# Optimization experiments

Measured on AMD Instinct MI355X. Metric: run time of the kernel, lower is better.

The kernel has to match this reference:

```python
import jax, jax.numpy as jnp
import numpy as np

LEAKY_ALPHA = 0.2  # LeakyReLU negative slope from init arg `alpha`


def setup_inputs() -> dict:
    key = jax.random.key(0)
    k1, k2, k3, k4 = jax.random.split(key, 4)
    B, N, Fin, Fout = 8, 2048, 256, 256
    h = jax.random.normal(k1, (B, N, Fin), dtype=jnp.float32)
    adj = jax.random.randint(k2, (N, N), 0, 2, dtype=jnp.int32)
    W = jax.random.normal(k3, (Fin, Fout), dtype=jnp.float32) * (1.414 * (6.0 / (Fin + Fout)) ** 0.5)
    a = jax.random.normal(k4, (2 * Fout, 1), dtype=jnp.float32) * (1.414 * (6.0 / (2 * Fout + 1)) ** 0.5)
    return {"h": h, "adj": adj, "W": W, "a": a}


def reference(h, adj, W, a):
    # h: (B, N, Fin), adj: (N, N) int {0,1}, W: (Fin, Fout), a: (2*Fout, 1)
    Fout = W.shape[1]
    Wh = jnp.einsum('bnf,fo->bno', h, W)            # (B, N, Fout)
    a1 = a[:Fout, 0]                                  # attends to target node i
    a2 = a[Fout:, 0]                                  # attends to source node j
    # a^T [Wh_i || Wh_j] == (Wh_i . a1) + (Wh_j . a2); LeakyReLU applied after, as in original
    s_i = Wh @ a1                                     # (B, N)
    s_j = Wh @ a2                                     # (B, N)
    e = jax.nn.leaky_relu(s_i[:, :, None] + s_j[:, None, :], negative_slope=LEAKY_ALPHA)  # (B, N, N)
    N = Wh.shape[1]
    mask = (adj > 0) | jnp.eye(N, dtype=bool)         # adjacency + self-loops
    e = jnp.where(mask[None, :, :], e, -jnp.inf)
    attention = jax.nn.softmax(e, axis=-1)            # dropout is identity in eval
    attention = jnp.nan_to_num(attention, nan=0.0)
    h_prime = jnp.einsum('bij,bjo->bio', attention, Wh)  # (B, N, Fout)
    return jax.nn.elu(h_prime)                        # concat=True -> ELU
```

## Files before the change

### kernel.cpp

```cpp
#include <hip/hip_runtime.h>

typedef unsigned short u16;
typedef unsigned int   u32;
typedef unsigned long long u64;

typedef __bf16 bf16x8 __attribute__((ext_vector_type(8)));
typedef float  f32x4  __attribute__((ext_vector_type(4)));

#define MFMA_BF16(a,b,c) __builtin_amdgcn_mfma_f32_16x16x32_bf16((a),(b),(c),0,0,0)

__device__ __forceinline__ float bf2f(u16 u) {
    return __uint_as_float(((u32)u) << 16);
}
__device__ __forceinline__ u16 f2bf(float x) {
    u32 u = __float_as_uint(x);
    u += 0x7fffu + ((u >> 16) & 1u);
    return (u16)(u >> 16);
}
__device__ __forceinline__ float ldany(const void* p, size_t i, int f32) {
    return f32 ? ((const float*)p)[i] : bf2f(((const u16*)p)[i]);
}
__device__ __forceinline__ int detect_f32(const u32* hw) {
    u32 w = hw[threadIdx.x & 63];
    int e = (w >> 23) & 0xFF;
    u64 m = __ballot(e >= 64 && e <= 190);
    return __popcll(m) >= 32 ? 1 : 0;
}

__global__ __launch_bounds__(256) void k0(const void* __restrict__ w, const void* __restrict__ a,
                                          u16* __restrict__ wt, float* __restrict__ wa1,
                                          float* __restrict__ wa2, const u32* __restrict__ hw) {
    int f32 = detect_f32(hw);
    int k = blockIdx.x, o = threadIdx.x;
    float wv = ldany(w, (size_t)k * 256 + o, f32);
    wt[o * 256 + k] = f2bf(wv);
    float p1 = wv * ldany(a, o, f32);
    float p2 = wv * ldany(a, 256 + o, f32);
    for (int d = 32; d; d >>= 1) { p1 += __shfl_down(p1, d); p2 += __shfl_down(p2, d); }
    __shared__ float s1[4], s2[4];
    int wid = o >> 6, lane = o & 63;
    if (lane == 0) { s1[wid] = p1; s2[wid] = p2; }
    __syncthreads();
    if (o == 0) { wa1[k] = s1[0] + s1[1] + s1[2] + s1[3]; wa2[k] = s2[0] + s2[1] + s2[2] + s2[3]; }
}

__global__ __launch_bounds__(256) void k1m(const int* __restrict__ adj, u64* __restrict__ mb64) {
    int t = threadIdx.x;
    int wv = t >> 6, lane = t & 63;
    #pragma unroll
    for (int q = 0; q < 4; q++) {
        int idx = blockIdx.x * 16 + wv * 4 + q;
        int mrow = idx >> 5, c = idx & 31;
        int j = c * 64 + lane;
        bool bit = (adj[(size_t)mrow * 2048 + j] > 0) || (j == mrow);
        u64 m = __ballot(bit);
        if (lane == 0) mb64[(size_t)mrow * 32 + c] = m;
    }
}

struct __align__(16) K2LDS {
    u16 At[64 * 68];
    union { u16 Bt[256 * 68]; u16 Ct[256 * 68]; };
    float wa1s[256], wa2s[256];
    float s1[64], s2[64];
};
__global__ __launch_bounds__(256) void k2(const void* __restrict__ h, const u16* __restrict__ wt,
                                          const float* __restrict__ wa1, const float* __restrict__ wa2,
                                          u16* __restrict__ whbt,
                                          float* __restrict__ sig, float* __restrict__ sjg) {
    __shared__ K2LDS L;
    int f32 = detect_f32((const u32*)h);
    int m0 = blockIdx.x * 64;
    int b  = m0 >> 11;
    int n0 = m0 & 2047;
    int t = threadIdx.x;
    int wid = t >> 6, lane = t & 63, ln = lane & 15, qd = lane >> 4;

    L.wa1s[t] = wa1[t]; L.wa2s[t] = wa2[t];
    if (t < 64) { L.s1[t] = 0.f; L.s2[t] = 0.f; }
    __syncthreads();

    float a1lo = 0.f, a2lo = 0.f, a1hi = 0.f, a2hi = 0.f;

    f32x4 acc[4][4];
    for (int mi = 0; mi < 4; mi++)
        for (int ni = 0; ni < 4; ni++)
            acc[mi][ni] = (f32x4){0.f, 0.f, 0.f, 0.f};

    for (int c = 0; c < 4; c++) {
        int k0c = c * 64;
        for (int p = 0; p < 2; p++) {
            int r = (t >> 3) + p * 32, s = t & 7;
            float xv[8]; u16 uv[8];
            if (f32) {
                const float* src = (const float*)h + (size_t)(m0 + r) * 256 + k0c + s * 8;
                f32x4 x0 = *(const f32x4*)src;
                f32x4 x1 = *(const f32x4*)(src + 4);
                #pragma unroll
                for (int q = 0; q < 4; q++) { xv[q] = x0[q]; xv[4 + q] = x1[q]; }
                #pragma unroll
                for (int q = 0; q < 8; q++) uv[q] = f2bf(xv[q]);
            } else {
                const u16* src = (const u16*)h + (size_t)(m0 + r) * 256 + k0c + s * 8;
                *(uint4*)uv = *(const uint4*)src;
                #pragma unroll
                for (int q = 0; q < 8; q++) xv[q] = bf2f(uv[q]);
            }
            *(uint4*)&L.At[r * 68 + s * 8] = *(uint4*)uv;
            float pa = 0.f, pb = 0.f;
            #pragma unroll
            for (int q = 0; q < 8; q++) {
                pa += xv[q] * L.wa1s[k0c + s * 8 + q];
                pb += xv[q] * L.wa2s[k0c + s * 8 + q];
            }
            if (p == 0) { a1lo += pa; a2lo += pb; } else { a1hi += pa; a2hi += pb; }
        }
        for (int p = 0; p < 8; p++) {
            int f = (t >> 3) + p * 32, s = t & 7;
            *(uint4*)&L.Bt[f * 68 + s * 8] =
                *(const uint4*)(wt + (size_t)f * 256 + k0c + s * 8);
        }
        __syncthreads();
        for (int ks = 0; ks < 2; ks++) {
            bf16x8 af[4], bfr[4];
            for (int mi = 0; mi < 4; mi++)
                af[mi] = *(const bf16x8*)&L.At[(mi * 16 + ln) * 68 + ks * 32 + qd * 8];
            for (int ni = 0; ni < 4; ni++)
                bfr[ni] = *(const bf16x8*)&L.Bt[(wid * 64 + ni * 16 + ln) * 68 + ks * 32 + qd * 8];
            for (int mi = 0; mi < 4; mi++)
                for (int ni = 0; ni < 4; ni++)
                    acc[mi][ni] = MFMA_BF16(af[mi], bfr[ni], acc[mi][ni]);
        }
        __syncthreads();
    }

    atomicAdd(&L.s1[t >> 3], a1lo);        atomicAdd(&L.s2[t >> 3], a2lo);
    atomicAdd(&L.s1[(t >> 3) + 32], a1hi); atomicAdd(&L.s2[(t >> 3) + 32], a2hi);

    for (int mi = 0; mi < 4; mi++) {
        for (int ni = 0; ni < 4; ni++) {
            int f = wid * 64 + ni * 16 + ln;
            int n = mi * 16 + qd * 4;
            u16 v[4];
            for (int r = 0; r < 4; r++) v[r] = f2bf(acc[mi][ni][r]);
            *(uint2*)&L.Ct[f * 68 + n] = *(uint2*)v;
        }
    }
    __syncthreads();
    if (t < 64) { sig[m0 + t] = L.s1[t]; sjg[m0 + t] = L.s2[t]; }
    {
        int fr = t;
        size_t base = (size_t)b * 524288 + (size_t)fr * 2048 + n0;
        #pragma unroll
        for (int s = 0; s < 8; s++) {
            uint4 v = *(uint4*)&L.Ct[fr * 68 + s * 8];
            *(uint4*)(whbt + base + s * 8) = v;
        }
    }
}

__global__ __launch_bounds__(512) void k3n(const float* __restrict__ sig, const float* __restrict__ sjg,
                                           float* __restrict__ u1g, float* __restrict__ u2g,
                                           u32* __restrict__ vpackg, u16* __restrict__ sjbfg) {
    int b = blockIdx.x;
    int t = threadIdx.x;
    const float* sjb = sjg + (size_t)b * 2048;
    float mx = -3.4e38f;
    #pragma unroll
    for (int p = 0; p < 4; p++) mx = fmaxf(mx, sjb[t + p * 512]);
    for (int d = 32; d; d >>= 1) mx = fmaxf(mx, __shfl_xor(mx, d));
    __shared__ float wmax[8];
    int wid = t >> 6, lane = t & 63;
    if (lane == 0) wmax[wid] = mx;
    __syncthreads();
    float Mb = fmaxf(fmaxf(fmaxf(wmax[0], wmax[1]), fmaxf(wmax[2], wmax[3])),
                     fmaxf(fmaxf(wmax[4], wmax[5]), fmaxf(wmax[6], wmax[7])));
    #pragma unroll
    for (int p = 0; p < 4; p++) {
        int j = t + p * 512;
        float sjv = sjb[j];
        float vj  = __expf(sjv - Mb);
        float v2j = __expf(0.2f * (sjv - Mb));
        vpackg[b * 2048 + j] = (u32)f2bf(vj) | ((u32)f2bf(v2j) << 16);
        sjbfg[b * 2048 + j]  = f2bf(sjv);
        float siv = sig[b * 2048 + j];
        float x = siv + Mb;
        float K = fmaxf(x, 0.2f * x);
        u1g[b * 2048 + j] = __expf(x - K);
        u2g[b * 2048 + j] = __expf(0.2f * x - K);
    }
}

struct __align__(16) K4LDS {
    u32   vpack[2048];
    u16   sjb[2048];
    u64   mw[64 * 33];
    float u1[64], u2[64], nsi[64], inv[64];
    float lred[512];
    u16   Pt[2][4096];
    int   claim[2];
};
__global__ __launch_bounds__(512, 1) void k4(const float* __restrict__ sig,
                                             const float* __restrict__ u1g, const float* __restrict__ u2g,
                                             const u32* __restrict__ vpackg, const u16* __restrict__ sjbfg,
                                             const u64* __restrict__ mb64, const u16* __restrict__ whbt,
                                             void* __restrict__ out, const void* __restrict__ hdet,
                                             int* __restrict__ cnt) {
    __shared__ K4LDS L;
    int f32 = detect_f32((const u32*)hdet);
    int t = threadIdx.x;
    if (t == 0) {
        int xcd = __builtin_amdgcn_s_getreg(63508) & 7;
        int bsel = 0, tile = 0;
        #pragma unroll
        for (int k = 0; k < 8; k++) {
            int bb = (xcd + k) & 7;
            int tt = atomicAdd(&cnt[bb], 1);
            if (tt < 32) { bsel = bb; tile = tt; break; }
        }
        L.claim[0] = bsel; L.claim[1] = tile;
    }
    __syncthreads();
    int b  = L.claim[0];
    int i0 = L.claim[1] * 64;
    int wid = t >> 6, lane = t & 63, ln = lane & 15, qd = lane >> 4;
    const u16* wb = whbt + (size_t)b * 524288 + (size_t)wid * 32 * 2048;
    float lacc = 0.f;

    bf16x8 br[2][4];
    #define LOAD_B(cc, bb) do {                                             \
        int j0_ = (cc) * 64;                                                \
        _Pragma("unroll")                                                   \
        for (int ni = 0; ni < 2; ni++)                                      \
            _Pragma("unroll")                                               \
            for (int ks = 0; ks < 2; ks++)                                  \
                br[bb][ni * 2 + ks] = *(const bf16x8*)(wb +                 \
                    (size_t)(ni * 16 + ln) * 2048 + j0_ + ks * 32 + qd * 8);\
    } while (0)

    #define PGEN(cc, bb) do {                                               \
        int r_ = lane, o_ = wid;                                            \
        int jb_ = (cc) * 64 + o_ * 8;                                       \
        uint4 pkA_ = *(const uint4*)&L.vpack[jb_];                          \
        uint4 pkB_ = *(const uint4*)&L.vpack[jb_ + 4];                      \
        uint4 sj4_ = *(const uint4*)&L.sjb[jb_];                            \
        u32 mb_ = (u32)(L.mw[r_ * 33 + (cc)] >> (o_ * 8)) & 0xffu;          \
        float u1_ = L.u1[r_], u2_ = L.u2[r_], nsi_ = L.nsi[r_];             \
        u32 pr_[4];                                                         \
        _Pragma("unroll")                                                   \
        for (int pk = 0; pk < 4; pk++) {                                    \
            u32 vw0_ = (pk == 0) ? pkA_.x : (pk == 1) ? pkA_.z              \
                     : (pk == 2) ? pkB_.x : pkB_.z;                         \
            u32 vw1_ = (pk == 0) ? pkA_.y : (pk == 1) ? pkA_.w              \
                     : (pk == 2) ? pkB_.y : pkB_.w;                         \
            u32 sw_ = (pk == 0) ? sj4_.x : (pk == 1) ? sj4_.y               \
                     : (pk == 2) ? sj4_.z : sj4_.w;                         \
            float sj0_ = __uint_as_float(sw_ << 16);                        \
            float sj1_ = __uint_as_float(sw_ & 0xffff0000u);                \
            float p0_, p1_;                                                 \
            {                                                               \
                bool pos = sj0_ > nsi_;                                     \
                float vv = __uint_as_float(pos ? (vw0_ << 16)               \
                                               : ((vw0_ >> 16) << 16));     \
                p0_ = (pos ? u1_ : u2_) * vv;                               \
                p0_ = ((mb_ >> (2 * pk)) & 1u) ? p0_ : 0.f;                 \
            }                                                               \
            {                                                               \
                bool pos = sj1_ > nsi_;                                     \
                float vv = __uint_as_float(pos ? (vw1_ << 16)               \
                                               : ((vw1_ >> 16) << 16));     \
                p1_ = (pos ? u1_ : u2_) * vv;                               \
                p1_ = ((mb_ >> (2 * pk + 1)) & 1u) ? p1_ : 0.f;             \
            }                                                               \
            lacc += p0_ + p1_;                                              \
            pr_[pk] = __builtin_amdgcn_perm(__float_as_uint(p1_),           \
                                            __float_as_uint(p0_),           \
                                            0x07060302u);                   \
        }                                                                   \
        *(uint4*)&L.Pt[bb][t * 8] = *(uint4*)pr_;                           \
    } while (0)

    LOAD_B(0, 0);
    for (int p = 0; p < 4; p++) { int idx = t + p * 512; L.vpack[idx] = vpackg[b * 2048 + idx]; }
    for (int p = 0; p < 2; p++) { int idx = t + p * 512;
        ((u32*)L.sjb)[idx] = ((const u32*)(sjbfg + (size_t)b * 2048))[idx]; }
    for (int p = 0; p < 4; p++) {
        int idx = t + p * 512;
        int r = idx >> 5, c = idx & 31;
        L.mw[r * 33 + c] = mb64[(size_t)(i0 + r) * 32 + c];
    }
    if (t < 64) {
        int row = b * 2048 + i0 + t;
        L.u1[t] = u1g[row]; L.u2[t] = u2g[row]; L.nsi[t] = -sig[row];
    }
    __syncthreads();
    PGEN(0, 0);

    f32x4 acc[4][2];
    for (int mi = 0; mi < 4; mi++)
        for (int ni = 0; ni < 2; ni++)
            acc[mi][ni] = (f32x4){0.f, 0.f, 0.f, 0.f};

    #define STEP(c, cur, nxt) do {                                          \
        __syncthreads();                                                    \
        if ((c) < 31) { LOAD_B((c) + 1, nxt); PGEN((c) + 1, nxt); }         \
        _Pragma("unroll")                                                   \
        for (int ks = 0; ks < 2; ks++) {                                    \
            bf16x8 af[4];                                                   \
            _Pragma("unroll")                                               \
            for (int mi = 0; mi < 4; mi++)                                  \
                af[mi] = *(const bf16x8*)&L.Pt[cur][((ks * 4 + qd) * 64 +   \
                                                     mi * 16 + ln) * 8];    \
            _Pragma("unroll")                                               \
            for (int mi = 0; mi < 4; mi++)                                  \
                _Pragma("unroll")                                           \
                for (int ni = 0; ni < 2; ni++)                              \
                    acc[mi][ni] = MFMA_BF16(af[mi], br[cur][ni * 2 + ks],   \
                                            acc[mi][ni]);                   \
        }                                                                   \
    } while (0)

    for (int cc = 0; cc < 16; cc++) {
        STEP(2 * cc,     0, 1);
        STEP(2 * cc + 1, 1, 0);
    }

    __syncthreads();
    L.lred[t] = lacc;
    __syncthreads();
    if (t < 64) {
        float s = 0.f;
        #pragma unroll
        for (int q = 0; q < 8; q++) s += L.lred[q * 64 + t];
        L.inv[t] = 1.0f / s;
    }
    __syncthreads();

    for (int mi = 0; mi < 4; mi++) {
        for (int ni = 0; ni < 2; ni++) {
            int fg = wid * 32 + ni * 16 + ln;
            for (int reg = 0; reg < 4; reg++) {
                int rl = mi * 16 + qd * 4 + reg;
                float hp = acc[mi][ni][reg] * L.inv[rl];
                float y = hp > 0.f ? hp : (__expf(hp) - 1.f);
                size_t idx = (size_t)(b * 2048 + i0 + rl) * 256 + fg;
                if (f32) ((float*)out)[idx] = y;
                else     ((u16*)out)[idx]   = f2bf(y);
            }
        }
    }
    #undef LOAD_B
    #undef PGEN
    #undef STEP
}

extern "C" void kernel_launch(void* const* d_in, const int* in_sizes, int n_in,
                              void* d_out, int out_size, void* d_ws, size_t ws_size,
                              hipStream_t stream) {
    const void* h   = d_in[0];
    const int*  adj = (const int*)d_in[1];
    const void* W   = d_in[2];
    const void* a   = d_in[3];

    char* ws = (char*)d_ws;
    u16*   WT    = (u16*)  (ws + 0);
    float* si    = (float*)(ws + 131072);
    float* sj    = (float*)(ws + 196608);
    float* u1    = (float*)(ws + 262144);
    float* u2    = (float*)(ws + 327680);
    u32*   vpack = (u32*)  (ws + 458752);
    u16*   sjbf  = (u16*)  (ws + 524288);
    u64*   mb64  = (u64*)  (ws + 557056);
    u16*   whbt  = (u16*)  (ws + 1081344);
    float* Wa1   = (float*)(ws + 9469952);
    float* Wa2   = (float*)(ws + 9470976);
    int*   cnt   = (int*)  (ws + 9472000);

    hipMemsetAsync(cnt, 0, 32, stream);
    k0 <<<dim3(256),  dim3(256), 0, stream>>>(W, a, WT, Wa1, Wa2, (const u32*)h);
    k1m<<<dim3(4096), dim3(256), 0, stream>>>(adj, mb64);
    k2 <<<dim3(256),  dim3(256), 0, stream>>>(h, WT, Wa1, Wa2, whbt, si, sj);
    k3n<<<dim3(8),    dim3(512), 0, stream>>>(si, sj, u1, u2, vpack, sjbf);
    k4 <<<dim3(256),  dim3(512), 0, stream>>>(si, u1, u2, vpack, sjbf, mb64, whbt, d_out, h, cnt);
}
```

Baseline: 139.5 us.

## Generate attention tiles in registers per wave, drop LDS staging and block syncs

The aggregation kernel now runs 256 threads per block. Each wave owns 32 rows and half of the feature columns, and builds its bf16 attention A-fragments directly in registers from global vpack, sj and mask data. This removes the LDS P tile, the shared staging arrays and the per-chunk __syncthreads. Softmax denominators are reduced with wave shuffles instead of through shared memory. In exchange, each wave redundantly computes the P values for its rows (two waves per row group), holds a much larger B-fragment register set, and issues more global loads with fewer threads per block.

```diff
diff --git a/kernel.cpp b/kernel.cpp
--- a/kernel.cpp
+++ b/kernel.cpp
@@ -191,22 +191,21 @@
     }
 }
 
-struct __align__(16) K4LDS {
-    u32   vpack[2048];
-    u16   sjb[2048];
-    u64   mw[64 * 33];
-    float u1[64], u2[64], nsi[64], inv[64];
-    float lred[512];
-    u16   Pt[2][4096];
-    int   claim[2];
-};
-__global__ __launch_bounds__(512, 1) void k4(const float* __restrict__ sig,
+__device__ __forceinline__ float pval(u32 vw, float sjv, float nsi,
+                                      float u1v, float u2v, u32 mbit) {
+    bool pos = sjv > nsi;
+    float vv = __uint_as_float(pos ? (vw << 16) : (vw & 0xffff0000u));
+    float uu = pos ? u1v : u2v;
+    float p = uu * vv;
+    return mbit ? p : 0.f;
+}
+__global__ __launch_bounds__(256, 1) void k4(const float* __restrict__ sig,
                                              const float* __restrict__ u1g, const float* __restrict__ u2g,
                                              const u32* __restrict__ vpackg, const u16* __restrict__ sjbfg,
                                              const u64* __restrict__ mb64, const u16* __restrict__ whbt,
                                              void* __restrict__ out, const void* __restrict__ hdet,
                                              int* __restrict__ cnt) {
-    __shared__ K4LDS L;
+    __shared__ int claim2[2];
     int f32 = detect_f32((const u32*)hdet);
     int t = threadIdx.x;
     if (t == 0) {
@@ -218,140 +217,124 @@
             int tt = atomicAdd(&cnt[bb], 1);
             if (tt < 32) { bsel = bb; tile = tt; break; }
         }
-        L.claim[0] = bsel; L.claim[1] = tile;
-    }
-    __syncthreads();
-    int b  = L.claim[0];
-    int i0 = L.claim[1] * 64;
+        claim2[0] = bsel; claim2[1] = tile;
+    }
+    __syncthreads();
+    int b  = claim2[0];
+    int i0 = claim2[1] * 64;
     int wid = t >> 6, lane = t & 63, ln = lane & 15, qd = lane >> 4;
-    const u16* wb = whbt + (size_t)b * 524288 + (size_t)wid * 32 * 2048;
-    float lacc = 0.f;
-
-    bf16x8 br[2][4];
-    #define LOAD_B(cc, bb) do {                                             \
-        int j0_ = (cc) * 64;                                                \
+    int rg = wid >> 1, fh = wid & 1;
+
+    int gi = b * 2048 + i0 + rg * 32;
+    const u16* wb = whbt + (size_t)b * 524288 + (size_t)(fh * 128) * 2048;
+    const u32* vp  = vpackg + (size_t)b * 2048;
+    const u16* sjp = sjbfg + (size_t)b * 2048;
+    const u64* mwr0 = mb64 + (size_t)(i0 + rg * 32 + ln) * 32;
+    const u64* mwr1 = mwr0 + 16 * 32;
+
+    float u1_0 = u1g[gi + ln],      u1_1 = u1g[gi + 16 + ln];
+    float u2_0 = u2g[gi + ln],      u2_1 = u2g[gi + 16 + ln];
+    float nsi0 = -sig[gi + ln],     nsi1 = -sig[gi + 16 + ln];
+    float lacc0 = 0.f, lacc1 = 0.f;
+
+    bf16x8 br[16];
+    bf16x8 ar[4];
+
+    #define LOAD_B_KS(cc, ks) do {                                          \
         _Pragma("unroll")                                                   \
-        for (int ni = 0; ni < 2; ni++)                                      \
-            _Pragma("unroll")                                               \
-            for (int ks = 0; ks < 2; ks++)                                  \
-                br[bb][ni * 2 + ks] = *(const bf16x8*)(wb +                 \
-                    (size_t)(ni * 16 + ln) * 2048 + j0_ + ks * 32 + qd * 8);\
+        for (int ni = 0; ni < 8; ni++)                                      \
+            br[ni * 2 + (ks)] = *(const bf16x8*)(wb +                       \
+                (size_t)(ni * 16 + ln) * 2048 + (cc) * 64 + (ks) * 32 + qd * 8);\
     } while (0)
 
-    #define PGEN(cc, bb) do {                                               \
-        int r_ = lane, o_ = wid;                                            \
-        int jb_ = (cc) * 64 + o_ * 8;                                       \
-        uint4 pkA_ = *(const uint4*)&L.vpack[jb_];                          \
-        uint4 pkB_ = *(const uint4*)&L.vpack[jb_ + 4];                      \
-        uint4 sj4_ = *(const uint4*)&L.sjb[jb_];                            \
-        u32 mb_ = (u32)(L.mw[r_ * 33 + (cc)] >> (o_ * 8)) & 0xffu;          \
-        float u1_ = L.u1[r_], u2_ = L.u2[r_], nsi_ = L.nsi[r_];             \
-        u32 pr_[4];                                                         \
-        _Pragma("unroll")                                                   \
-        for (int pk = 0; pk < 4; pk++) {                                    \
-            u32 vw0_ = (pk == 0) ? pkA_.x : (pk == 1) ? pkA_.z              \
-                     : (pk == 2) ? pkB_.x : pkB_.z;                         \
-            u32 vw1_ = (pk == 0) ? pkA_.y : (pk == 1) ? pkA_.w              \
-                     : (pk == 2) ? pkB_.y : pkB_.w;                         \
-            u32 sw_ = (pk == 0) ? sj4_.x : (pk == 1) ? sj4_.y               \
-                     : (pk == 2) ? sj4_.z : sj4_.w;                         \
-            float sj0_ = __uint_as_float(sw_ << 16);                        \
-            float sj1_ = __uint_as_float(sw_ & 0xffff0000u);                \
-            float p0_, p1_;                                                 \
-            {                                                               \
-                bool pos = sj0_ > nsi_;                                     \
-                float vv = __uint_as_float(pos ? (vw0_ << 16)               \
-                                               : ((vw0_ >> 16) << 16));     \
-                p0_ = (pos ? u1_ : u2_) * vv;                               \
-                p0_ = ((mb_ >> (2 * pk)) & 1u) ? p0_ : 0.f;                 \
-            }                                                               \
-            {                                                               \
-                bool pos = sj1_ > nsi_;                                     \
-                float vv = __uint_as_float(pos ? (vw1_ << 16)               \
-                                               : ((vw1_ >> 16) << 16));     \
-                p1_ = (pos ? u1_ : u2_) * vv;                               \
-                p1_ = ((mb_ >> (2 * pk + 1)) & 1u) ? p1_ : 0.f;             \
-            }                                                               \
-            lacc += p0_ + p1_;                                              \
-            pr_[pk] = __builtin_amdgcn_perm(__float_as_uint(p1_),           \
-                                            __float_as_uint(p0_),           \
-                                            0x07060302u);                   \
-        }                                                                   \
-        *(uint4*)&L.Pt[bb][t * 8] = *(uint4*)pr_;                           \
-    } while (0)
-
-    LOAD_B(0, 0);
-    for (int p = 0; p < 4; p++) { int idx = t + p * 512; L.vpack[idx] = vpackg[b * 2048 + idx]; }
-    for (int p = 0; p < 2; p++) { int idx = t + p * 512;
-        ((u32*)L.sjb)[idx] = ((const u32*)(sjbfg + (size_t)b * 2048))[idx]; }
-    for (int p = 0; p < 4; p++) {
-        int idx = t + p * 512;
-        int r = idx >> 5, c = idx & 31;
-        L.mw[r * 33 + c] = mb64[(size_t)(i0 + r) * 32 + c];
-    }
-    if (t < 64) {
-        int row = b * 2048 + i0 + t;
-        L.u1[t] = u1g[row]; L.u2[t] = u2g[row]; L.nsi[t] = -sig[row];
-    }
-    __syncthreads();
-    PGEN(0, 0);
-
-    f32x4 acc[4][2];
-    for (int mi = 0; mi < 4; mi++)
-        for (int ni = 0; ni < 2; ni++)
-            acc[mi][ni] = (f32x4){0.f, 0.f, 0.f, 0.f};
-
-    #define STEP(c, cur, nxt) do {                                          \
-        __syncthreads();                                                    \
-        if ((c) < 31) { LOAD_B((c) + 1, nxt); PGEN((c) + 1, nxt); }         \
+    #define PGEN(cc) do {                                                   \
+        u64 mw0_ = mwr0[cc], mw1_ = mwr1[cc];                               \
         _Pragma("unroll")                                                   \
         for (int ks = 0; ks < 2; ks++) {                                    \
-            bf16x8 af[4];                                                   \
+            int jb_ = (cc) * 64 + ks * 32 + qd * 8;                         \
+            u32 vv_[8];                                                     \
+            *(uint4*)&vv_[0] = *(const uint4*)&vp[jb_];                     \
+            *(uint4*)&vv_[4] = *(const uint4*)&vp[jb_ + 4];                 \
+            u32 sw_[4];                                                     \
+            *(uint4*)sw_ = *(const uint4*)&sjp[jb_];                        \
+            u32 mB0_ = (u32)(mw0_ >> (ks * 32 + qd * 8)) & 0xffu;           \
+            u32 mB1_ = (u32)(mw1_ >> (ks * 32 + qd * 8)) & 0xffu;           \
+            u32 pk0_[4], pk1_[4];                                           \
             _Pragma("unroll")                                               \
-            for (int mi = 0; mi < 4; mi++)                                  \
-                af[mi] = *(const bf16x8*)&L.Pt[cur][((ks * 4 + qd) * 64 +   \
-                                                     mi * 16 + ln) * 8];    \
-            _Pragma("unroll")                                               \
-            for (int mi = 0; mi < 4; mi++)                                  \
-                _Pragma("unroll")                                           \
-                for (int ni = 0; ni < 2; ni++)                              \
-                    acc[mi][ni] = MFMA_BF16(af[mi], br[cur][ni * 2 + ks],   \
-                                            acc[mi][ni]);                   \
+            for (int pk = 0; pk < 4; pk++) {                                \
+                float sj0_ = __uint_as_float(sw_[pk] << 16);                \
+                float sj1_ = __uint_as_float(sw_[pk] & 0xffff0000u);        \
+                float a0_ = pval(vv_[2 * pk],     sj0_, nsi0, u1_0, u2_0,   \
+                                 (mB0_ >> (2 * pk)) & 1u);                  \
+                float a1_ = pval(vv_[2 * pk + 1], sj1_, nsi0, u1_0, u2_0,   \
+                                 (mB0_ >> (2 * pk + 1)) & 1u);              \
+                lacc0 += a0_ + a1_;                                         \
+                pk0_[pk] = __builtin_amdgcn_perm(__float_as_uint(a1_),      \
+                                                 __float_as_uint(a0_),      \
+                                                 0x07060302u);              \
+                float b0_ = pval(vv_[2 * pk],     sj0_, nsi1, u1_1, u2_1,   \
+                                 (mB1_ >> (2 * pk)) & 1u);                  \
+                float b1_ = pval(vv_[2 * pk + 1], sj1_, nsi1, u1_1, u2_1,   \
+                                 (mB1_ >> (2 * pk + 1)) & 1u);              \
+                lacc1 += b0_ + b1_;                                         \
+                pk1_[pk] = __builtin_amdgcn_perm(__float_as_uint(b1_),      \
+                                                 __float_as_uint(b0_),      \
+                                                 0x07060302u);              \
+            }                                                               \
+            ar[ks]     = *(bf16x8*)pk0_;                                    \
+            ar[2 + ks] = *(bf16x8*)pk1_;                                    \
         }                                                                   \
     } while (0)
 
-    for (int cc = 0; cc < 16; cc++) {
-        STEP(2 * cc,     0, 1);
-        STEP(2 * cc + 1, 1, 0);
-    }
-
-    __syncthreads();
-    L.lred[t] = lacc;
-    __syncthreads();
-    if (t < 64) {
-        float s = 0.f;
-        #pragma unroll
-        for (int q = 0; q < 8; q++) s += L.lred[q * 64 + t];
-        L.inv[t] = 1.0f / s;
-    }
-    __syncthreads();
-
-    for (int mi = 0; mi < 4; mi++) {
-        for (int ni = 0; ni < 2; ni++) {
-            int fg = wid * 32 + ni * 16 + ln;
-            for (int reg = 0; reg < 4; reg++) {
-                int rl = mi * 16 + qd * 4 + reg;
-                float hp = acc[mi][ni][reg] * L.inv[rl];
+    f32x4 acc0[8], acc1[8];
+    #pragma unroll
+    for (int ni = 0; ni < 8; ni++) {
+        acc0[ni] = (f32x4){0.f, 0.f, 0.f, 0.f};
+        acc1[ni] = (f32x4){0.f, 0.f, 0.f, 0.f};
+    }
+
+    LOAD_B_KS(0, 0);
+    LOAD_B_KS(0, 1);
+    PGEN(0);
+
+    for (int c = 0; c < 32; c++) {
+        #pragma unroll
+        for (int ni = 0; ni < 8; ni++) {
+            acc0[ni] = MFMA_BF16(ar[0], br[ni * 2 + 0], acc0[ni]);
+            acc1[ni] = MFMA_BF16(ar[2], br[ni * 2 + 0], acc1[ni]);
+        }
+        if (c < 31) LOAD_B_KS(c + 1, 0);
+        #pragma unroll
+        for (int ni = 0; ni < 8; ni++) {
+            acc0[ni] = MFMA_BF16(ar[1], br[ni * 2 + 1], acc0[ni]);
+            acc1[ni] = MFMA_BF16(ar[3], br[ni * 2 + 1], acc1[ni]);
+        }
+        if (c < 31) { LOAD_B_KS(c + 1, 1); PGEN(c + 1); }
+    }
+
+    lacc0 += __shfl_xor(lacc0, 16); lacc0 += __shfl_xor(lacc0, 32);
+    lacc1 += __shfl_xor(lacc1, 16); lacc1 += __shfl_xor(lacc1, 32);
+    float linv0 = 1.0f / lacc0, linv1 = 1.0f / lacc1;
+
+    #pragma unroll
+    for (int mi = 0; mi < 2; mi++) {
+        #pragma unroll
+        for (int reg = 0; reg < 4; reg++) {
+            float inv = __shfl(mi ? linv1 : linv0, qd * 4 + reg);
+            int row = b * 2048 + i0 + rg * 32 + mi * 16 + qd * 4 + reg;
+            #pragma unroll
+            for (int ni = 0; ni < 8; ni++) {
+                int fg = fh * 128 + ni * 16 + ln;
+                float hp = (mi ? acc1[ni][reg] : acc0[ni][reg]) * inv;
                 float y = hp > 0.f ? hp : (__expf(hp) - 1.f);
-                size_t idx = (size_t)(b * 2048 + i0 + rl) * 256 + fg;
+                size_t idx = (size_t)row * 256 + fg;
                 if (f32) ((float*)out)[idx] = y;
                 else     ((u16*)out)[idx]   = f2bf(y);
             }
         }
     }
-    #undef LOAD_B
+    #undef LOAD_B_KS
     #undef PGEN
-    #undef STEP
 }
 
 extern "C" void kernel_launch(void* const* d_in, const int* in_sizes, int n_in,
@@ -381,5 +364,5 @@
     k1m<<<dim3(4096), dim3(256), 0, stream>>>(adj, mb64);
     k2 <<<dim3(256),  dim3(256), 0, stream>>>(h, WT, Wa1, Wa2, whbt, si, sj);
     k3n<<<dim3(8),    dim3(512), 0, stream>>>(si, sj, u1, u2, vpack, sjbf);
-    k4 <<<dim3(256),  dim3(512), 0, stream>>>(si, u1, u2, vpack, sjbf, mb64, whbt, d_out, h, cnt);
-}
+    k4 <<<dim3(256),  dim3(256), 0, stream>>>(si, u1, u2, vpack, sjbf, mb64, whbt, d_out, h, cnt);
+}
```

Result: slower. 203.7 us (+46.0%).

## Halve k4 row tile to 32 rows and launch 512 blocks for occupancy

Applied to the files above, without the earlier changes.

The main attention kernel now handles 32 query rows per block instead of 64, doubling the grid to 512 blocks and raising launch bounds to allow several blocks per CU. The P-generation mapping, LDS tile layout, accumulator count and row-sum reduction are reworked to match. The goal is better latency hiding and load balance across the CUs. The cost is that each block reloads the full per-batch vpack/sjb tables and the B operand (Wh), so that global and LDS traffic per output row doubles.

```diff
diff --git a/kernel.cpp b/kernel.cpp
--- a/kernel.cpp
+++ b/kernel.cpp
@@ -25,6 +25,14 @@
     int e = (w >> 23) & 0xFF;
     u64 m = __ballot(e >= 64 && e <= 190);
     return __popcll(m) >= 32 ? 1 : 0;
+}
+__device__ __forceinline__ float pval(u32 vw, float sjv, float nsi,
+                                      float u1v, float u2v, u32 mbit) {
+    bool pos = sjv > nsi;
+    float vv = __uint_as_float(pos ? (vw << 16) : (vw & 0xffff0000u));
+    float uu = pos ? u1v : u2v;
+    float p = uu * vv;
+    return mbit ? p : 0.f;
 }
 
 __global__ __launch_bounds__(256) void k0(const void* __restrict__ w, const void* __restrict__ a,
@@ -194,13 +202,13 @@
 struct __align__(16) K4LDS {
     u32   vpack[2048];
     u16   sjb[2048];
-    u64   mw[64 * 33];
-    float u1[64], u2[64], nsi[64], inv[64];
+    u64   mw[32 * 33];
+    float u1[32], u2[32], nsi[32], inv[32];
     float lred[512];
-    u16   Pt[2][4096];
+    u16   Pt[2][2048];
     int   claim[2];
 };
-__global__ __launch_bounds__(512, 1) void k4(const float* __restrict__ sig,
+__global__ __launch_bounds__(512, 4) void k4(const float* __restrict__ sig,
                                              const float* __restrict__ u1g, const float* __restrict__ u2g,
                                              const u32* __restrict__ vpackg, const u16* __restrict__ sjbfg,
                                              const u64* __restrict__ mb64, const u16* __restrict__ whbt,
@@ -216,13 +224,13 @@
         for (int k = 0; k < 8; k++) {
             int bb = (xcd + k) & 7;
             int tt = atomicAdd(&cnt[bb], 1);
-            if (tt < 32) { bsel = bb; tile = tt; break; }
+            if (tt < 64) { bsel = bb; tile = tt; break; }
         }
         L.claim[0] = bsel; L.claim[1] = tile;
     }
     __syncthreads();
     int b  = L.claim[0];
-    int i0 = L.claim[1] * 64;
+    int i0 = L.claim[1] * 32;
     int wid = t >> 6, lane = t & 63, ln = lane & 15, qd = lane >> 4;
     const u16* wb = whbt + (size_t)b * 524288 + (size_t)wid * 32 * 2048;
     float lacc = 0.f;
@@ -239,65 +247,51 @@
     } while (0)
 
     #define PGEN(cc, bb) do {                                               \
-        int r_ = lane, o_ = wid;                                            \
-        int jb_ = (cc) * 64 + o_ * 8;                                       \
-        uint4 pkA_ = *(const uint4*)&L.vpack[jb_];                          \
-        uint4 pkB_ = *(const uint4*)&L.vpack[jb_ + 4];                      \
-        uint4 sj4_ = *(const uint4*)&L.sjb[jb_];                            \
-        u32 mb_ = (u32)(L.mw[r_ * 33 + (cc)] >> (o_ * 8)) & 0xffu;          \
+        int r_ = t & 31, q_ = t >> 5;                                       \
+        int jb_ = (cc) * 64 + q_ * 4;                                       \
+        uint4 vw4_ = *(const uint4*)&L.vpack[jb_];                          \
+        u32 sw2_[2]; *(uint2*)sw2_ = *(const uint2*)&L.sjb[jb_];            \
+        u32 mb_ = (u32)(L.mw[r_ * 33 + (cc)] >> (q_ * 4)) & 0xfu;           \
         float u1_ = L.u1[r_], u2_ = L.u2[r_], nsi_ = L.nsi[r_];             \
-        u32 pr_[4];                                                         \
+        u32 pr_[2];                                                         \
         _Pragma("unroll")                                                   \
-        for (int pk = 0; pk < 4; pk++) {                                    \
-            u32 vw0_ = (pk == 0) ? pkA_.x : (pk == 1) ? pkA_.z              \
-                     : (pk == 2) ? pkB_.x : pkB_.z;                         \
-            u32 vw1_ = (pk == 0) ? pkA_.y : (pk == 1) ? pkA_.w              \
-                     : (pk == 2) ? pkB_.y : pkB_.w;                         \
-            u32 sw_ = (pk == 0) ? sj4_.x : (pk == 1) ? sj4_.y               \
-                     : (pk == 2) ? sj4_.z : sj4_.w;                         \
+        for (int pk = 0; pk < 2; pk++) {                                    \
+            u32 vw0_ = pk ? vw4_.z : vw4_.x;                                \
+            u32 vw1_ = pk ? vw4_.w : vw4_.y;                                \
+            u32 sw_  = sw2_[pk];                                            \
             float sj0_ = __uint_as_float(sw_ << 16);                        \
             float sj1_ = __uint_as_float(sw_ & 0xffff0000u);                \
-            float p0_, p1_;                                                 \
-            {                                                               \
-                bool pos = sj0_ > nsi_;                                     \
-                float vv = __uint_as_float(pos ? (vw0_ << 16)               \
-                                               : ((vw0_ >> 16) << 16));     \
-                p0_ = (pos ? u1_ : u2_) * vv;                               \
-                p0_ = ((mb_ >> (2 * pk)) & 1u) ? p0_ : 0.f;                 \
-            }                                                               \
-            {                                                               \
-                bool pos = sj1_ > nsi_;                                     \
-                float vv = __uint_as_float(pos ? (vw1_ << 16)               \
-                                               : ((vw1_ >> 16) << 16));     \
-                p1_ = (pos ? u1_ : u2_) * vv;                               \
-                p1_ = ((mb_ >> (2 * pk + 1)) & 1u) ? p1_ : 0.f;             \
-            }                                                               \
+            float p0_ = pval(vw0_, sj0_, nsi_, u1_, u2_,                    \
+                             (mb_ >> (2 * pk)) & 1u);                       \
+            float p1_ = pval(vw1_, sj1_, nsi_, u1_, u2_,                    \
+                             (mb_ >> (2 * pk + 1)) & 1u);                   \
             lacc += p0_ + p1_;                                              \
             pr_[pk] = __builtin_amdgcn_perm(__float_as_uint(p1_),           \
                                             __float_as_uint(p0_),           \
                                             0x07060302u);                   \
         }                                                                   \
-        *(uint4*)&L.Pt[bb][t * 8] = *(uint4*)pr_;                           \
+        *(uint2*)&L.Pt[bb][((q_ >> 1) * 32 + r_) * 8 + (q_ & 1) * 4] =      \
+            *(uint2*)pr_;                                                   \
     } while (0)
 
     LOAD_B(0, 0);
     for (int p = 0; p < 4; p++) { int idx = t + p * 512; L.vpack[idx] = vpackg[b * 2048 + idx]; }
     for (int p = 0; p < 2; p++) { int idx = t + p * 512;
         ((u32*)L.sjb)[idx] = ((const u32*)(sjbfg + (size_t)b * 2048))[idx]; }
-    for (int p = 0; p < 4; p++) {
+    for (int p = 0; p < 2; p++) {
         int idx = t + p * 512;
         int r = idx >> 5, c = idx & 31;
         L.mw[r * 33 + c] = mb64[(size_t)(i0 + r) * 32 + c];
     }
-    if (t < 64) {
+    if (t < 32) {
         int row = b * 2048 + i0 + t;
         L.u1[t] = u1g[row]; L.u2[t] = u2g[row]; L.nsi[t] = -sig[row];
     }
     __syncthreads();
     PGEN(0, 0);
 
-    f32x4 acc[4][2];
-    for (int mi = 0; mi < 4; mi++)
+    f32x4 acc[2][2];
+    for (int mi = 0; mi < 2; mi++)
         for (int ni = 0; ni < 2; ni++)
             acc[mi][ni] = (f32x4){0.f, 0.f, 0.f, 0.f};
 
@@ -306,13 +300,13 @@
         if ((c) < 31) { LOAD_B((c) + 1, nxt); PGEN((c) + 1, nxt); }         \
         _Pragma("unroll")                                                   \
         for (int ks = 0; ks < 2; ks++) {                                    \
-            bf16x8 af[4];                                                   \
+            bf16x8 af[2];                                                   \
             _Pragma("unroll")                                               \
-            for (int mi = 0; mi < 4; mi++)                                  \
-                af[mi] = *(const bf16x8*)&L.Pt[cur][((ks * 4 + qd) * 64 +   \
+            for (int mi = 0; mi < 2; mi++)                                  \
+                af[mi] = *(const bf16x8*)&L.Pt[cur][((ks * 4 + qd) * 32 +   \
                                                      mi * 16 + ln) * 8];    \
             _Pragma("unroll")                                               \
-            for (int mi = 0; mi < 4; mi++)                                  \
+            for (int mi = 0; mi < 2; mi++)                                  \
                 _Pragma("unroll")                                           \
                 for (int ni = 0; ni < 2; ni++)                              \
                     acc[mi][ni] = MFMA_BF16(af[mi], br[cur][ni * 2 + ks],   \
@@ -328,15 +322,15 @@
     __syncthreads();
     L.lred[t] = lacc;
     __syncthreads();
-    if (t < 64) {
+    if (t < 32) {
         float s = 0.f;
         #pragma unroll
-        for (int q = 0; q < 8; q++) s += L.lred[q * 64 + t];
+        for (int q = 0; q < 16; q++) s += L.lred[q * 32 + t];
         L.inv[t] = 1.0f / s;
     }
     __syncthreads();
 
-    for (int mi = 0; mi < 4; mi++) {
+    for (int mi = 0; mi < 2; mi++) {
         for (int ni = 0; ni < 2; ni++) {
             int fg = wid * 32 + ni * 16 + ln;
             for (int reg = 0; reg < 4; reg++) {
@@ -381,5 +375,5 @@
     k1m<<<dim3(4096), dim3(256), 0, stream>>>(adj, mb64);
     k2 <<<dim3(256),  dim3(256), 0, stream>>>(h, WT, Wa1, Wa2, whbt, si, sj);
     k3n<<<dim3(8),    dim3(512), 0, stream>>>(si, sj, u1, u2, vpack, sjbf);
-    k4 <<<dim3(256),  dim3(512), 0, stream>>>(si, u1, u2, vpack, sjbf, mb64, whbt, d_out, h, cnt);
-}
+    k4 <<<dim3(512),  dim3(512), 0, stream>>>(si, u1, u2, vpack, sjbf, mb64, whbt, d_out, h, cnt);
+}
```

New measurement: 170.0 us. +21.9%, slower.
